# Kernel tuning notes

Hardware: AMD Instinct MI355X
Metric: run time of the kernel (lower is better)

The kernel has to match this reference:

```python
import jax, jax.numpy as jnp
import numpy as np

B, L, D = 4, 4096, 1024
H = 16
HD = D // H                      # 64
WIN = 256
MLP_RATIO = 4.0
FFN = int(2 * int(D * MLP_RATIO) / 3)   # 2730
EPS = 1e-6


def setup_inputs() -> dict:
    key = jax.random.key(0)
    ks = jax.random.split(key, 16)
    s = 0.02
    return {
        "x": jax.random.normal(ks[0], (B, L, D), jnp.float32),
        "c": jax.random.normal(ks[1], (B, D), jnp.float32),
        "norm1_scale": jnp.ones((D,), jnp.float32),
        "norm2_scale": jnp.ones((D,), jnp.float32),
        "adaLN_w": jax.random.normal(ks[2], (D, 6 * D), jnp.float32) * s,
        "adaLN_b": jnp.zeros((6 * D,), jnp.float32),
        "qkv_w": jax.random.normal(ks[3], (D, 3 * D), jnp.float32) * s,
        "qkv_b": jnp.zeros((3 * D,), jnp.float32),
        "out_proj_w": jax.random.normal(ks[4], (D, D), jnp.float32) * s,
        "out_proj_b": jnp.zeros((D,), jnp.float32),
        "w12_w": jax.random.normal(ks[5], (D, 2 * FFN), jnp.float32) * s,
        "w12_b": jnp.zeros((2 * FFN,), jnp.float32),
        "w3_w": jax.random.normal(ks[6], (FFN, D), jnp.float32) * s,
        "w3_b": jnp.zeros((D,), jnp.float32),
    }


def _rmsnorm(x, scale):
    xf = x.astype(jnp.float32)
    var = jnp.mean(jnp.square(xf), axis=-1, keepdims=True)
    xn = (xf * jax.lax.rsqrt(var + EPS)).astype(x.dtype)
    return xn * scale


def _modulation(x, shift, scale):
    return x * (1.0 + scale[:, None, :]) + shift[:, None, :]


def _rope(x):
    # Faithful to original: seq axis is x.shape[-2], which here is the HEAD axis.
    seq_len, hd = x.shape[-2], x.shape[-1]
    theta = 10000.0
    freqs = 1.0 / theta ** (jnp.arange(0, hd, 2, dtype=jnp.float32) / hd)
    t = jnp.arange(seq_len, dtype=jnp.float32)
    freqs_cis = jnp.einsum("i,j->ij", t, freqs)        # (seq, hd/2)
    sin = jnp.repeat(jnp.sin(freqs_cis), 2, axis=-1)   # (seq, hd)
    cos = jnp.repeat(jnp.cos(freqs_cis), 2, axis=-1)
    x1, x2 = jnp.split(x, 2, axis=-1)
    rot = jnp.concatenate([-x2, x1], axis=-1)
    return x * cos + rot * sin


def reference(x, c, norm1_scale, norm2_scale, adaLN_w, adaLN_b,
              qkv_w, qkv_b, out_proj_w, out_proj_b,
              w12_w, w12_b, w3_w, w3_b):
    # adaLN modulation params from conditioning
    ada = jax.nn.silu(c) @ adaLN_w + adaLN_b                      # (B, 6D)
    sh_msa, sc_msa, g_msa, sh_mlp, sc_mlp, g_mlp = jnp.split(ada, 6, axis=-1)

    # --- attention branch ---
    res = x
    xm = _modulation(_rmsnorm(x, norm1_scale), sh_msa, sc_msa)    # (B,L,D)
    nw = L // WIN
    xw = xm.reshape(B * nw, WIN, D)
    qkv = xw @ qkv_w + qkv_b
    q, k, v = jnp.split(qkv, 3, axis=-1)
    q = q.reshape(B * nw, WIN, H, HD)
    k = k.reshape(B * nw, WIN, H, HD)
    v = v.reshape(B * nw, WIN, H, HD)
    q, k = _rope(q), _rope(k)
    scores = jnp.einsum("bqhd,bkhd->bhqk", q, k) / jnp.sqrt(jnp.float32(HD))
    attn = jax.nn.softmax(scores, axis=-1)
    out = jnp.einsum("bhqk,bkhd->bqhd", attn, v).reshape(B, L, D)
    out = out @ out_proj_w + out_proj_b
    x = res + g_msa[:, None, :] * out

    # --- MLP branch ---
    res = x
    xm = _modulation(_rmsnorm(x, norm2_scale), sh_mlp, sc_mlp)
    w12 = xm @ w12_w + w12_b                                      # (B,L,2*FFN)
    w1, w2 = jnp.split(w12, 2, axis=-1)
    mlp = (jax.nn.silu(w1) * w2) @ w3_w + w3_b
    return res + g_mlp[:, None, :] * mlp
```

## Files before the change

### kernel.cpp

```cpp
#include <hip/hip_runtime.h>
#include <hip/hip_bf16.h>
#include <cstdint>
#include <cstddef>

#define DEV __device__ __forceinline__

typedef float f32x4 __attribute__((ext_vector_type(4)));
typedef short s16x8 __attribute__((ext_vector_type(8)));
typedef short s16x4 __attribute__((ext_vector_type(4)));
typedef __bf16 bf16x8 __attribute__((ext_vector_type(8)));

DEV unsigned short f2bf(float f) {
  union { float f; unsigned u; } v; v.f = f;
  return (unsigned short)((v.u + 0x7FFFu + ((v.u >> 16) & 1u)) >> 16);
}
DEV float bf2f(unsigned short s) {
  union { unsigned u; float f; } v; v.u = ((unsigned)s) << 16;
  return v.f;
}

DEV void mfma16(f32x4& d, const s16x8& a, const s16x8& b) {
  d = __builtin_amdgcn_mfma_f32_16x16x32_bf16(
      __builtin_bit_cast(bf16x8, a), __builtin_bit_cast(bf16x8, b), d, 0, 0, 0);
}

typedef const unsigned int gu32 __attribute__((address_space(1)));
typedef unsigned int lu32 __attribute__((address_space(3)));
DEV void gl_lds16(const void* g, void* l) {
  __builtin_amdgcn_global_load_lds((gu32*)g, (lu32*)l, 16, 0, 0);
}

__global__ void transpose_w(const float* __restrict__ src, int srcLd, int K,
                            int colOff, int nCols,
                            unsigned short* __restrict__ dst, int dstLd, int rowOff,
                            int ilv)
{
  __shared__ float tile[32][33];
  int tx = threadIdx.x & 31, ty = threadIdx.x >> 5;
  int k0 = blockIdx.y * 32, n0 = blockIdx.x * 32;
#pragma unroll
  for (int r = 0; r < 4; ++r) {
    int kk = k0 + ty + r * 8;
    int nn = n0 + tx;
    if (kk < K && nn < nCols) tile[ty + r * 8][tx] = src[(size_t)kk * srcLd + colOff + nn];
  }
  __syncthreads();
#pragma unroll
  for (int r = 0; r < 4; ++r) {
    int nn = n0 + ty + r * 8;
    int kk = k0 + tx;
    if (nn < nCols && kk < K) {
      int row = ilv ? (((nn >> 4) << 5) + (nn & 15) + rowOff) : (rowOff + nn);
      dst[(size_t)row * dstLd + kk] = f2bf(tile[tx][ty + r * 8]);
    }
  }
}

__global__ void biaspad_kernel(const float* __restrict__ b, float* __restrict__ out)
{
  int n = blockIdx.x * 256 + threadIdx.x;
  if (n >= 5632) return;
  int bb = n >> 4, i = n & 15;
  int src = ((bb >> 1) << 4) + i;
  float v = 0.f;
  if (src < 2730) v = (bb & 1) ? b[2730 + src] : b[src];
  out[n] = v;
}

__global__ void ada_kernel(const float* __restrict__ c, const float* __restrict__ w,
                           const float* __restrict__ b, float* __restrict__ ada)
{
  __shared__ float cs[1024];
  int bb = blockIdx.y;
  int j = blockIdx.x * 256 + threadIdx.x;
  for (int i = threadIdx.x; i < 1024; i += 256) {
    float v = c[bb * 1024 + i];
    cs[i] = v / (1.f + __expf(-v));
  }
  __syncthreads();
  float acc = b[j];
  for (int k = 0; k < 1024; ++k) acc = fmaf(cs[k], w[(size_t)k * 6144 + j], acc);
  ada[bb * 6144 + j] = acc;
}

__global__ void rmsmod_kernel(const float* __restrict__ x, const float* __restrict__ nsc,
                              const float* __restrict__ ada, int shOff, int scOff,
                              unsigned short* __restrict__ out)
{
  int row = blockIdx.x;
  int t = threadIdx.x;
  const f32x4* xr = (const f32x4*)(x + (size_t)row * 1024);
  f32x4 v = xr[t];
  float ss = v[0]*v[0] + v[1]*v[1] + v[2]*v[2] + v[3]*v[3];
#pragma unroll
  for (int off = 32; off >= 1; off >>= 1) ss += __shfl_xor(ss, off, 64);
  __shared__ float red[4];
  int lane = t & 63, wv = t >> 6;
  if (lane == 0) red[wv] = ss;
  __syncthreads();
  float tot = red[0] + red[1] + red[2] + red[3];
  float rms = rsqrtf(tot * (1.f / 1024.f) + 1e-6f);
  int bb = row >> 12;
  const float* ab = ada + bb * 6144;
  s16x4 o;
#pragma unroll
  for (int i = 0; i < 4; ++i) {
    int col = t * 4 + i;
    float xn = v[i] * rms * nsc[col];
    float val = xn * (1.f + ab[scOff + col]) + ab[shOff + col];
    o[i] = (short)f2bf(val);
  }
  *(s16x4*)(out + (size_t)row * 1024 + t * 4) = o;
}

template<int EPI>
__global__ __launch_bounds__(512, 2) void gemm256(
    const unsigned short* __restrict__ A, int lda,
    const unsigned short* __restrict__ BT, int ldb,
    int N, int K,
    const float* __restrict__ bias,
    void* __restrict__ Cout, int Nout,
    const float* __restrict__ res,
    const float* __restrict__ ada, int gateOff,
    unsigned short* __restrict__ vTout)
{
  __shared__ __align__(16) char lds[131072];

  const int tid = threadIdx.x;
  const int lane = tid & 63;
  const int wv = tid >> 6;
  const int wr = wv >> 2;
  const int wn = wv & 3;
  const int g = lane >> 4, r16 = lane & 15;

  const int nwg = gridDim.x * gridDim.y;
  const int bid = blockIdx.x + gridDim.x * blockIdx.y;
  const int qq = nwg >> 3;
  const int swz = (bid & 7) * qq + (bid >> 3);
  const int m0 = (swz / gridDim.x) * 256;
  const int n0 = (swz % gridDim.x) * 256;

  const int nkt = K >> 6;

  auto stageB = [&](int t) {
    if (t >= nkt) return;
    const int bs = t & 1;
#pragma unroll
    for (int it = 0; it < 4; ++it) {
      const int cidx = it * 512 + tid;
      const int rl = cidx >> 3, cc = cidx & 7;
      const unsigned short* src =
          BT + (size_t)(n0 + rl) * ldb + t * 64 + ((cc ^ (rl & 7)) << 3);
      gl_lds16(src, lds + 65536 + bs * 32768 + cidx * 16);
    }
  };
  auto stageA = [&](int t) {
    if (t >= nkt) return;
    const int bs = t & 1;
#pragma unroll
    for (int it = 0; it < 4; ++it) {
      const int cidx = it * 512 + tid;
      const int rl = cidx >> 3, cc = cidx & 7;
      const unsigned short* src =
          A + (size_t)(m0 + rl) * lda + t * 64 + ((cc ^ (rl & 7)) << 3);
      gl_lds16(src, lds + bs * 32768 + cidx * 16);
    }
  };

  f32x4 acc[8][4];
#pragma unroll
  for (int m = 0; m < 8; ++m)
#pragma unroll
    for (int n = 0; n < 4; ++n) { acc[m][n][0]=0.f; acc[m][n][1]=0.f; acc[m][n][2]=0.f; acc[m][n][3]=0.f; }

  int swzk[2];
#pragma unroll
  for (int ks = 0; ks < 2; ++ks) swzk[ks] = (((ks << 2) + g) ^ (r16 & 7)) << 4;
  int arow0[4], arow1[4], brow0[2], brow1[2];
#pragma unroll
  for (int m = 0; m < 4; ++m) {
    arow0[m] = (wr * 128 + m * 16 + r16) * 128;
    arow1[m] = (wr * 128 + 64 + m * 16 + r16) * 128;
  }
#pragma unroll
  for (int n = 0; n < 2; ++n) {
    brow0[n] = 65536 + (wn * 64 + n * 16 + r16) * 128;
    brow1[n] = 65536 + (wn * 64 + 32 + n * 16 + r16) * 128;
  }

  stageB(0); stageA(0); stageB(1); stageA(1);
  asm volatile("s_waitcnt vmcnt(8)" ::: "memory");
  __builtin_amdgcn_s_barrier();

  for (int kt = 0; kt < nkt; ++kt) {
    const int boff = (kt & 1) * 32768;
    s16x8 a0[4][2], a1[4][2], b0[2][2], b1[2][2];
#pragma unroll
    for (int m = 0; m < 4; ++m)
#pragma unroll
      for (int ks = 0; ks < 2; ++ks)
        a0[m][ks] = *(const s16x8*)(lds + boff + arow0[m] + swzk[ks]);
#pragma unroll
    for (int n = 0; n < 2; ++n)
#pragma unroll
      for (int ks = 0; ks < 2; ++ks)
        b0[n][ks] = *(const s16x8*)(lds + boff + brow0[n] + swzk[ks]);
#pragma unroll
    for (int n = 0; n < 2; ++n)
#pragma unroll
      for (int ks = 0; ks < 2; ++ks)
        b1[n][ks] = *(const s16x8*)(lds + boff + brow1[n] + swzk[ks]);
#pragma unroll
    for (int m = 0; m < 4; ++m)
#pragma unroll
      for (int ks = 0; ks < 2; ++ks)
        a1[m][ks] = *(const s16x8*)(lds + boff + arow1[m] + swzk[ks]);
    __builtin_amdgcn_s_setprio(1);
#pragma unroll
    for (int m = 0; m < 4; ++m)
#pragma unroll
      for (int n = 0; n < 2; ++n)
#pragma unroll
        for (int ks = 0; ks < 2; ++ks)
          mfma16(acc[m][n], a0[m][ks], b0[n][ks]);
    __builtin_amdgcn_s_setprio(0);
    __builtin_amdgcn_s_setprio(1);
#pragma unroll
    for (int m = 0; m < 4; ++m)
#pragma unroll
      for (int n = 0; n < 2; ++n)
#pragma unroll
        for (int ks = 0; ks < 2; ++ks)
          mfma16(acc[m][2 + n], a0[m][ks], b1[n][ks]);
    __builtin_amdgcn_s_setprio(0);
    __builtin_amdgcn_s_barrier();
    stageB(kt + 2);
    __builtin_amdgcn_s_setprio(1);
#pragma unroll
    for (int m = 0; m < 4; ++m)
#pragma unroll
      for (int n = 0; n < 2; ++n)
#pragma unroll
        for (int ks = 0; ks < 2; ++ks)
          mfma16(acc[4 + m][2 + n], a1[m][ks], b1[n][ks]);
    __builtin_amdgcn_s_setprio(0);
    if (kt + 2 < nkt) asm volatile("s_waitcnt vmcnt(4)" ::: "memory");
    else              asm volatile("s_waitcnt vmcnt(0)" ::: "memory");
    __builtin_amdgcn_s_barrier();
    stageA(kt + 2);
    __builtin_amdgcn_s_setprio(1);
#pragma unroll
    for (int m = 0; m < 4; ++m)
#pragma unroll
      for (int n = 0; n < 2; ++n)
#pragma unroll
        for (int ks = 0; ks < 2; ++ks)
          mfma16(acc[4 + m][n], a1[m][ks], b0[n][ks]);
    __builtin_amdgcn_s_setprio(0);
  }

  if (EPI == 1) {
    unsigned short* Co = (unsigned short*)Cout;
#pragma unroll
    for (int fm = 0; fm < 8; ++fm)
#pragma unroll
      for (int p = 0; p < 2; ++p)
#pragma unroll
        for (int r = 0; r < 4; ++r) {
          int rg = m0 + wr * 128 + fm * 16 + g * 4 + r;
          int cg = n0 + wn * 64 + (2 * p) * 16 + r16;
          float v1 = acc[fm][2 * p][r] + bias[cg];
          float v2 = acc[fm][2 * p + 1][r] + bias[cg + 16];
          float h = v1 / (1.f + __expf(-v1)) * v2;
          int hcol = (n0 >> 1) + wn * 32 + p * 16 + r16;
          Co[(size_t)rg * Nout + hcol] = f2bf(h);
        }
  } else if (EPI == 2) {
    float* Co = (float*)Cout;
#pragma unroll
    for (int fm = 0; fm < 8; ++fm)
#pragma unroll
      for (int fn = 0; fn < 4; ++fn)
#pragma unroll
        for (int r = 0; r < 4; ++r) {
          int rg = m0 + wr * 128 + fm * 16 + g * 4 + r;
          int cg = n0 + wn * 64 + fn * 16 + r16;
          float v = acc[fm][fn][r] + bias[cg];
          int bb = rg >> 12;
          float gate = ada[bb * 6144 + gateOff + cg];
          size_t idx = (size_t)rg * Nout + cg;
          Co[idx] = res[idx] + gate * v;
        }
  } else {
    unsigned short* Co = (unsigned short*)Cout;
#pragma unroll
    for (int fn = 0; fn < 4; ++fn) {
      int cg = n0 + wn * 64 + fn * 16 + r16;
      float bs = bias[cg];
      if (n0 + wn * 64 + fn * 16 < 2048) {
#pragma unroll
        for (int fm = 0; fm < 8; ++fm)
#pragma unroll
          for (int r = 0; r < 4; ++r) {
            int rg = m0 + wr * 128 + fm * 16 + g * 4 + r;
            Co[(size_t)rg * Nout + cg] = f2bf(acc[fm][fn][r] + bs);
          }
      } else {
        int h = (cg - 2048) >> 6, d = (cg - 2048) & 63;
        unsigned short* vcol = vTout + (size_t)h * 16384 + d * 256;
#pragma unroll
        for (int fm = 0; fm < 8; ++fm)
#pragma unroll
          for (int r = 0; r < 4; ++r) {
            int rg = m0 + wr * 128 + fm * 16 + g * 4 + r;
            vcol[((size_t)(rg >> 8) * 16) * 16384 + (rg & 255)] =
                f2bf(acc[fm][fn][r] + bs);
          }
      }
    }
  }
}

template<int MODE>
__global__ void gemm128(const unsigned short* __restrict__ A, int lda,
                        const unsigned short* __restrict__ BT,
                        int N, int K,
                        const float* __restrict__ bias,
                        void* __restrict__ Cout,
                        const float* __restrict__ res,
                        const float* __restrict__ ada, int gateOff, int mOff)
{
  __shared__ __align__(16) unsigned short As[128 * 32];
  __shared__ __align__(16) unsigned short Bs[128 * 32];

  const int tid = threadIdx.x;
  const int lane = tid & 63;
  const int wv = tid >> 6;
  const int wr = wv >> 1, wc = wv & 1;
  const int g = lane >> 4, r16 = lane & 15;
  const int m0 = blockIdx.y * 128, n0 = blockIdx.x * 128;

  const int c0 = tid, c1 = 256 + tid;
  const int ra0 = c0 >> 2, ra1 = c1 >> 2;
  const int k0 = ((c0 & 3) ^ ((ra0 >> 1) & 3)) * 8;
  const int k1 = ((c1 & 3) ^ ((ra1 >> 1) & 3)) * 8;
  const unsigned short* ga0 = A + (size_t)(m0 + ra0) * lda + k0;
  const unsigned short* ga1 = A + (size_t)(m0 + ra1) * lda + k1;
  const unsigned short* gb0 = BT + (size_t)(n0 + ra0) * K + k0;
  const unsigned short* gb1 = BT + (size_t)(n0 + ra1) * K + k1;
  unsigned short* la0 = As + c0 * 8;
  unsigned short* la1 = As + c1 * 8;
  unsigned short* lb0 = Bs + c0 * 8;
  unsigned short* lb1 = Bs + c1 * 8;

  f32x4 acc[4][4];
#pragma unroll
  for (int m = 0; m < 4; ++m)
#pragma unroll
    for (int n = 0; n < 4; ++n) { acc[m][n][0]=0.f; acc[m][n][1]=0.f; acc[m][n][2]=0.f; acc[m][n][3]=0.f; }

  int aoff[4], boff[4];
#pragma unroll
  for (int m = 0; m < 4; ++m) {
    int rl = wr * 64 + m * 16 + r16;
    aoff[m] = rl * 32 + (g ^ ((rl >> 1) & 3)) * 8;
    int rb = wc * 64 + m * 16 + r16;
    boff[m] = rb * 32 + (g ^ ((rb >> 1) & 3)) * 8;
  }

  const int nk = K >> 5;
  for (int kt = 0; kt < nk; ++kt) {
    __syncthreads();
    const int ko = kt * 32;
    gl_lds16(ga0 + ko, la0);
    gl_lds16(ga1 + ko, la1);
    gl_lds16(gb0 + ko, lb0);
    gl_lds16(gb1 + ko, lb1);
    __syncthreads();
    s16x8 af[4], bf[4];
#pragma unroll
    for (int m = 0; m < 4; ++m) af[m] = *(const s16x8*)(As + aoff[m]);
#pragma unroll
    for (int n = 0; n < 4; ++n) bf[n] = *(const s16x8*)(Bs + boff[n]);
#pragma unroll
    for (int m = 0; m < 4; ++m)
#pragma unroll
      for (int n = 0; n < 4; ++n) mfma16(acc[m][n], af[m], bf[n]);
  }

#pragma unroll
  for (int m = 0; m < 4; ++m) {
#pragma unroll
    for (int n = 0; n < 4; ++n) {
#pragma unroll
      for (int r = 0; r < 4; ++r) {
        int rg = m0 + wr * 64 + m * 16 + g * 4 + r;
        int cg = n0 + wc * 64 + n * 16 + r16;
        float v = acc[m][n][r] + bias[cg];
        size_t idx = (size_t)rg * N + cg;
        if (MODE == 0 || MODE == 2) {
          ((unsigned short*)Cout)[idx] = f2bf(v);
        } else {
          int bb = (mOff + rg) >> 12;
          float gate = ada[bb * 6144 + gateOff + cg];
          ((float*)Cout)[idx] = res[idx] + gate * v;
        }
      }
    }
  }
}

__global__ __launch_bounds__(256, 1) void attn_kernel(
    const unsigned short* __restrict__ qkv,
    const unsigned short* __restrict__ vT,
    unsigned short* __restrict__ attnout)
{
  __shared__ __align__(16) unsigned short Kl[256 * 64];
  __shared__ __align__(16) unsigned short Vl[64 * 256];
  __shared__ __align__(16) unsigned short Pl[4][64 * 88];

  const int tid = threadIdx.x;
  const int lane = tid & 63;
  const int wv = tid >> 6;
  const int g = lane >> 4, r16 = lane & 15;
  const int p = blockIdx.x;
  const int w = p >> 4, h = p & 15;
  const float hh = (float)h;
  const float F = 0.4152410118609203f;

#pragma unroll
  for (int it = 0; it < 4; ++it) {
    int idx = it * 256 + tid;
    int j = idx >> 2;
    int c = idx & 3;
    const unsigned short* kg = qkv + (size_t)(w * 256 + j) * 3072 + 1024 + h * 64;
    s16x8 lo = *(const s16x8*)(kg + c * 8);
    s16x8 hi = *(const s16x8*)(kg + 32 + c * 8);
    s16x8 plo, phi;
#pragma unroll
    for (int i2 = 0; i2 < 4; ++i2) {
      float f1 = exp2f(-(float)(c * 4 + i2) * F);
      float f2 = exp2f(-(float)(16 + c * 4 + i2) * F);
      float s1, c1s, s2, c2s;
      sincosf(hh * f1, &s1, &c1s);
      sincosf(hh * f2, &s2, &c2s);
#pragma unroll
      for (int u = 0; u < 2; ++u) {
        int i = i2 * 2 + u;
        float a = bf2f((unsigned short)lo[i]);
        float b = bf2f((unsigned short)hi[i]);
        plo[i] = (short)f2bf(a * c1s - b * s1);
        phi[i] = (short)f2bf(b * c2s + a * s2);
      }
    }
    int swzL = c ^ (j & 7);
    int swzH = (c + 4) ^ (j & 7);
    *(s16x8*)(Kl + j * 64 + swzL * 8) = plo;
    *(s16x8*)(Kl + j * 64 + swzH * 8) = phi;
  }
  {
    const unsigned short* vg = vT + (size_t)p * (64 * 256);
#pragma unroll
    for (int it = 0; it < 8; ++it) {
      int idx = it * 256 + tid;
      int d = idx >> 5;
      int c = idx & 31;
      s16x8 val = *(const s16x8*)(vg + d * 256 + c * 8);
      int cs = (c & ~7) | ((c ^ d) & 7);
      *(s16x8*)(Vl + d * 256 + cs * 8) = val;
    }
  }

  s16x8 qa[4][2];
  {
    float cs0[4], sn0[4], cs1[4], sn1[4];
#pragma unroll
    for (int i2 = 0; i2 < 4; ++i2) {
      float f1 = exp2f(-(float)(g * 4 + i2) * F);
      float f2 = exp2f(-(float)(16 + g * 4 + i2) * F);
      sincosf(hh * f1, &sn0[i2], &cs0[i2]);
      sincosf(hh * f2, &sn1[i2], &cs1[i2]);
    }
#pragma unroll
    for (int m = 0; m < 4; ++m) {
      const unsigned short* qg =
          qkv + (size_t)(w * 256 + wv * 64 + m * 16 + r16) * 3072 + h * 64;
      s16x8 lo = *(const s16x8*)(qg + g * 8);
      s16x8 hi = *(const s16x8*)(qg + 32 + g * 8);
      s16x8 plo, phi;
#pragma unroll
      for (int i = 0; i < 8; ++i) {
        int i2 = i >> 1;
        float a = bf2f((unsigned short)lo[i]);
        float b = bf2f((unsigned short)hi[i]);
        plo[i] = (short)f2bf(a * cs0[i2] - b * sn0[i2]);
        phi[i] = (short)f2bf(b * cs1[i2] + a * sn1[i2]);
      }
      qa[m][0] = plo;
      qa[m][1] = phi;
    }
  }

  __syncthreads();

  f32x4 accO[4][4];
  float Mx[4][4], Ls[4][4];
#pragma unroll
  for (int m = 0; m < 4; ++m)
#pragma unroll
    for (int r = 0; r < 4; ++r) {
      Mx[m][r] = -3.0e38f;
      Ls[m][r] = 0.f;
      accO[m][r][0]=0.f; accO[m][r][1]=0.f; accO[m][r][2]=0.f; accO[m][r][3]=0.f;
    }
  unsigned short* Pw = &Pl[wv][0];
  const float zs = 0.125f * 1.44269504f;

  for (int kb = 0; kb < 4; ++kb) {
    f32x4 s[4][4];
#pragma unroll
    for (int m = 0; m < 4; ++m)
#pragma unroll
      for (int jt = 0; jt < 4; ++jt) { s[m][jt][0]=0.f; s[m][jt][1]=0.f; s[m][jt][2]=0.f; s[m][jt][3]=0.f; }

#pragma unroll
    for (int jt = 0; jt < 4; ++jt) {
      int j = kb * 64 + jt * 16 + r16;
      s16x8 bk0 = *(const s16x8*)(Kl + j * 64 + ((g ^ (j & 7)) * 8));
      s16x8 bk1 = *(const s16x8*)(Kl + j * 64 + (((4 + g) ^ (j & 7)) * 8));
#pragma unroll
      for (int m = 0; m < 4; ++m) {
        mfma16(s[m][jt], qa[m][0], bk0);
        mfma16(s[m][jt], qa[m][1], bk1);
      }
    }

#pragma unroll
    for (int m = 0; m < 4; ++m) {
#pragma unroll
      for (int r = 0; r < 4; ++r) {
        float mx = fmaxf(fmaxf(s[m][0][r], s[m][1][r]), fmaxf(s[m][2][r], s[m][3][r]));
        mx = fmaxf(mx, __shfl_xor(mx, 1, 16));
        mx = fmaxf(mx, __shfl_xor(mx, 2, 16));
        mx = fmaxf(mx, __shfl_xor(mx, 4, 16));
        mx = fmaxf(mx, __shfl_xor(mx, 8, 16));
        float Mn = fmaxf(Mx[m][r], mx * zs);
        float fsc = exp2f(Mx[m][r] - Mn);
        Mx[m][r] = Mn;
        float ps = 0.f;
#pragma unroll
        for (int jt = 0; jt < 4; ++jt) {
          float pv = exp2f(s[m][jt][r] * zs - Mn);
          s[m][jt][r] = pv;
          ps += pv;
        }
        ps += __shfl_xor(ps, 1, 16);
        ps += __shfl_xor(ps, 2, 16);
        ps += __shfl_xor(ps, 4, 16);
        ps += __shfl_xor(ps, 8, 16);
        Ls[m][r] = Ls[m][r] * fsc + ps;
#pragma unroll
        for (int dt = 0; dt < 4; ++dt) accO[m][dt][r] *= fsc;
      }
    }

#pragma unroll
    for (int m = 0; m < 4; ++m)
#pragma unroll
      for (int jt = 0; jt < 4; ++jt)
#pragma unroll
        for (int r = 0; r < 4; ++r) {
          int q = m * 16 + g * 4 + r;
          int jj = jt * 16 + r16;
          Pw[q * 88 + jj] = f2bf(s[m][jt][r]);
        }
    asm volatile("s_waitcnt lgkmcnt(0)" ::: "memory");
    __builtin_amdgcn_sched_barrier(0);

#pragma unroll
    for (int c = 0; c < 2; ++c) {
      s16x8 pa[4];
#pragma unroll
      for (int m = 0; m < 4; ++m)
        pa[m] = *(const s16x8*)(Pw + (m * 16 + r16) * 88 + c * 32 + g * 8);
#pragma unroll
      for (int dt = 0; dt < 4; ++dt) {
        int d = dt * 16 + r16;
        int cch = kb * 8 + c * 4 + g;
        int csz = (cch & ~7) | ((cch ^ d) & 7);
        s16x8 vb = *(const s16x8*)(Vl + d * 256 + csz * 8);
#pragma unroll
        for (int m = 0; m < 4; ++m) mfma16(accO[m][dt], pa[m], vb);
      }
    }
    asm volatile("s_waitcnt lgkmcnt(0)" ::: "memory");
    __builtin_amdgcn_sched_barrier(0);
  }

#pragma unroll
  for (int m = 0; m < 4; ++m)
#pragma unroll
    for (int dt = 0; dt < 4; ++dt)
#pragma unroll
      for (int r = 0; r < 4; ++r) {
        int rg = w * 256 + wv * 64 + m * 16 + g * 4 + r;
        int cg = h * 64 + dt * 16 + r16;
        float val = accO[m][dt][r] / Ls[m][r];
        attnout[(size_t)rg * 1024 + cg] = f2bf(val);
      }
}

extern "C" void kernel_launch(void* const* d_in, const int* in_sizes, int n_in,
                              void* d_out, int out_size, void* d_ws, size_t ws_size,
                              hipStream_t stream)
{
  const float* x    = (const float*)d_in[0];
  const float* c    = (const float*)d_in[1];
  const float* n1s  = (const float*)d_in[2];
  const float* n2s  = (const float*)d_in[3];
  const float* adaW = (const float*)d_in[4];
  const float* adaB = (const float*)d_in[5];
  const float* qkvW = (const float*)d_in[6];
  const float* qkvB = (const float*)d_in[7];
  const float* outW = (const float*)d_in[8];
  const float* outB = (const float*)d_in[9];
  const float* w12W = (const float*)d_in[10];
  const float* w12B = (const float*)d_in[11];
  const float* w3W  = (const float*)d_in[12];
  const float* w3B  = (const float*)d_in[13];

  char* ws = (char*)d_ws;
  constexpr size_t OFF_ADA  = 0;
  constexpr size_t OFF_QKVT = 98304;
  constexpr size_t OFF_OUTT = OFF_QKVT + 6291456;
  constexpr size_t OFF_W12T = OFF_OUTT + 2097152;
  constexpr size_t OFF_W3T  = OFF_W12T + 11534336;
  constexpr size_t OFF_BPAD = OFF_W3T + 5767168;
  constexpr size_t OFF_XM   = OFF_BPAD + 22528;
  constexpr size_t OFF_BIG  = OFF_XM + 33554432;
  constexpr size_t OFF_QKVC = OFF_BIG;
  constexpr size_t OFF_VTC  = OFF_BIG + 50331648;
  constexpr size_t OFF_ATTC = OFF_BIG + 67108864;
  constexpr size_t OFF_HBUF = OFF_BIG;

  float* ada            = (float*)(ws + OFF_ADA);
  unsigned short* qkvT  = (unsigned short*)(ws + OFF_QKVT);
  unsigned short* outT  = (unsigned short*)(ws + OFF_OUTT);
  unsigned short* w12T  = (unsigned short*)(ws + OFF_W12T);
  unsigned short* w3T   = (unsigned short*)(ws + OFF_W3T);
  float* biasPad        = (float*)(ws + OFF_BPAD);
  unsigned short* xm    = (unsigned short*)(ws + OFF_XM);
  unsigned short* qkvbC = (unsigned short*)(ws + OFF_QKVC);
  unsigned short* vTbC  = (unsigned short*)(ws + OFF_VTC);
  unsigned short* attnC = (unsigned short*)(ws + OFF_ATTC);
  unsigned short* hbuf  = (unsigned short*)(ws + OFF_HBUF);
  float* x2             = (float*)d_out;

  hipMemsetAsync(w12T, 0, 11534336, stream);
  hipMemsetAsync(w3T, 0, 5767168, stream);
  transpose_w<<<dim3(96, 32), 256, 0, stream>>>(qkvW, 3072, 1024, 0, 3072, qkvT, 1024, 0, 0);
  transpose_w<<<dim3(32, 32), 256, 0, stream>>>(outW, 1024, 1024, 0, 1024, outT, 1024, 0, 0);
  transpose_w<<<dim3(86, 32), 256, 0, stream>>>(w12W, 5460, 1024, 0, 2730, w12T, 1024, 0, 1);
  transpose_w<<<dim3(86, 32), 256, 0, stream>>>(w12W, 5460, 1024, 2730, 2730, w12T, 1024, 16, 1);
  transpose_w<<<dim3(32, 86), 256, 0, stream>>>(w3W, 1024, 2730, 0, 1024, w3T, 2816, 0, 0);
  biaspad_kernel<<<22, 256, 0, stream>>>(w12B, biasPad);
  ada_kernel<<<dim3(24, 4), 256, 0, stream>>>(c, adaW, adaB, ada);

  rmsmod_kernel<<<16384, 256, 0, stream>>>(x, n1s, ada, 0, 1024, xm);
  for (int ch = 0; ch < 2; ++ch) {
    const size_t ro = (size_t)ch * 8192;
    gemm256<3><<<dim3(12, 32), 512, 0, stream>>>(
        xm + ro * 1024, 1024, qkvT, 1024, 3072, 1024, qkvB, qkvbC, 3072,
        nullptr, nullptr, 0, vTbC);
    attn_kernel<<<512, 256, 0, stream>>>(qkvbC, vTbC, attnC);
    gemm128<1><<<dim3(8, 64), 256, 0, stream>>>(
        attnC, 1024, outT, 1024, 1024, outB, x2 + ro * 1024, x + ro * 1024,
        ada, 2048, (int)ro);
  }

  rmsmod_kernel<<<16384, 256, 0, stream>>>(x2, n2s, ada, 3072, 4096, xm);
  gemm256<1><<<dim3(22, 64), 512, 0, stream>>>(
      xm, 1024, w12T, 1024, 5632, 1024, biasPad, hbuf, 2816,
      nullptr, nullptr, 0, nullptr);
  gemm256<2><<<dim3(4, 64), 512, 0, stream>>>(
      hbuf, 2816, w3T, 2816, 1024, 2816, w3B, x2, 1024,
      x2, ada, 5120, nullptr);
}
```

Before: 765.9 us.

## Interleave LDS fragment reads and global staging with MFMA phases in GEMM loop

Restructures the GEMM main loop so the b1 and a1 LDS fragment loads happen just before the MFMA phase that uses them, rather than all up front. Each phase is bracketed by barriers and lgkmcnt waits. Global-to-LDS staging is split into two 128-row halves, and the vmcnt wait moves to the end of each iteration. The aim is to cut register pressure and overlap LDS and global traffic with matrix work. The cost is several extra workgroup barriers per K-step, which could stall the waves.

```diff
diff --git a/kernel.cpp b/kernel.cpp
--- a/kernel.cpp
+++ b/kernel.cpp
@@ -142,28 +142,30 @@
 
   const int nkt = K >> 6;
 
-  auto stageB = [&](int t) {
+  auto stageBh = [&](int t, int h) {
     if (t >= nkt) return;
     const int bs = t & 1;
 #pragma unroll
-    for (int it = 0; it < 4; ++it) {
+    for (int it = 0; it < 2; ++it) {
       const int cidx = it * 512 + tid;
       const int rl = cidx >> 3, cc = cidx & 7;
+      const int row = h * 128 + rl;
       const unsigned short* src =
-          BT + (size_t)(n0 + rl) * ldb + t * 64 + ((cc ^ (rl & 7)) << 3);
-      gl_lds16(src, lds + 65536 + bs * 32768 + cidx * 16);
+          BT + (size_t)(n0 + row) * ldb + t * 64 + ((cc ^ (rl & 7)) << 3);
+      gl_lds16(src, lds + 65536 + bs * 32768 + h * 16384 + cidx * 16);
     }
   };
-  auto stageA = [&](int t) {
+  auto stageAh = [&](int t, int h) {
     if (t >= nkt) return;
     const int bs = t & 1;
 #pragma unroll
-    for (int it = 0; it < 4; ++it) {
+    for (int it = 0; it < 2; ++it) {
       const int cidx = it * 512 + tid;
       const int rl = cidx >> 3, cc = cidx & 7;
+      const int row = h * 128 + rl;
       const unsigned short* src =
-          A + (size_t)(m0 + rl) * lda + t * 64 + ((cc ^ (rl & 7)) << 3);
-      gl_lds16(src, lds + bs * 32768 + cidx * 16);
+          A + (size_t)(m0 + row) * lda + t * 64 + ((cc ^ (rl & 7)) << 3);
+      gl_lds16(src, lds + bs * 32768 + h * 16384 + cidx * 16);
     }
   };
 
@@ -188,7 +190,8 @@
     brow1[n] = 65536 + (wn * 64 + 32 + n * 16 + r16) * 128;
   }
 
-  stageB(0); stageA(0); stageB(1); stageA(1);
+  stageBh(0, 0); stageBh(0, 1); stageAh(0, 0); stageAh(0, 1);
+  stageBh(1, 0); stageBh(1, 1); stageAh(1, 0); stageAh(1, 1);
   asm volatile("s_waitcnt vmcnt(8)" ::: "memory");
   __builtin_amdgcn_s_barrier();
 
@@ -205,16 +208,8 @@
 #pragma unroll
       for (int ks = 0; ks < 2; ++ks)
         b0[n][ks] = *(const s16x8*)(lds + boff + brow0[n] + swzk[ks]);
-#pragma unroll
-    for (int n = 0; n < 2; ++n)
-#pragma unroll
-      for (int ks = 0; ks < 2; ++ks)
-        b1[n][ks] = *(const s16x8*)(lds + boff + brow1[n] + swzk[ks]);
-#pragma unroll
-    for (int m = 0; m < 4; ++m)
-#pragma unroll
-      for (int ks = 0; ks < 2; ++ks)
-        a1[m][ks] = *(const s16x8*)(lds + boff + arow1[m] + swzk[ks]);
+    __builtin_amdgcn_s_barrier();
+    asm volatile("s_waitcnt lgkmcnt(0)" ::: "memory");
     __builtin_amdgcn_s_setprio(1);
 #pragma unroll
     for (int m = 0; m < 4; ++m)
@@ -224,6 +219,14 @@
         for (int ks = 0; ks < 2; ++ks)
           mfma16(acc[m][n], a0[m][ks], b0[n][ks]);
     __builtin_amdgcn_s_setprio(0);
+    __builtin_amdgcn_s_barrier();
+#pragma unroll
+    for (int n = 0; n < 2; ++n)
+#pragma unroll
+      for (int ks = 0; ks < 2; ++ks)
+        b1[n][ks] = *(const s16x8*)(lds + boff + brow1[n] + swzk[ks]);
+    __builtin_amdgcn_s_barrier();
+    asm volatile("s_waitcnt lgkmcnt(0)" ::: "memory");
     __builtin_amdgcn_s_setprio(1);
 #pragma unroll
     for (int m = 0; m < 4; ++m)
@@ -234,7 +237,15 @@
           mfma16(acc[m][2 + n], a0[m][ks], b1[n][ks]);
     __builtin_amdgcn_s_setprio(0);
     __builtin_amdgcn_s_barrier();
-    stageB(kt + 2);
+#pragma unroll
+    for (int m = 0; m < 4; ++m)
+#pragma unroll
+      for (int ks = 0; ks < 2; ++ks)
+        a1[m][ks] = *(const s16x8*)(lds + boff + arow1[m] + swzk[ks]);
+    stageBh(kt + 2, 0);
+    stageBh(kt + 2, 1);
+    __builtin_amdgcn_s_barrier();
+    asm volatile("s_waitcnt lgkmcnt(0)" ::: "memory");
     __builtin_amdgcn_s_setprio(1);
 #pragma unroll
     for (int m = 0; m < 4; ++m)
@@ -244,10 +255,10 @@
         for (int ks = 0; ks < 2; ++ks)
           mfma16(acc[4 + m][2 + n], a1[m][ks], b1[n][ks]);
     __builtin_amdgcn_s_setprio(0);
-    if (kt + 2 < nkt) asm volatile("s_waitcnt vmcnt(4)" ::: "memory");
-    else              asm volatile("s_waitcnt vmcnt(0)" ::: "memory");
     __builtin_amdgcn_s_barrier();
-    stageA(kt + 2);
+    stageAh(kt + 2, 0);
+    stageAh(kt + 2, 1);
+    __builtin_amdgcn_s_barrier();
     __builtin_amdgcn_s_setprio(1);
 #pragma unroll
     for (int m = 0; m < 4; ++m)
@@ -257,6 +268,8 @@
         for (int ks = 0; ks < 2; ++ks)
           mfma16(acc[4 + m][n], a1[m][ks], b0[n][ks]);
     __builtin_amdgcn_s_setprio(0);
+    asm volatile("s_waitcnt vmcnt(8)" ::: "memory");
+    __builtin_amdgcn_s_barrier();
   }
 
   if (EPI == 1) {
```

After: 805.7 us. 5.2% more time.

## Shrink gemm256 tile to 256x128 with K-step 32 for higher occupancy

Applied to the files above, without the earlier changes.

Reworks the main bf16 GEMM from a 256x256 tile with K-step 64 to a 256x128 tile with K-step 32. The wave layout changes to 4x2, each wave holds a 64x64 accumulator, and LDS drops from 128KB to 48KB. The launch bound rises to 4 blocks per CU and grid widths double. The goal is more resident workgroups and better wave balance across CUs, at the cost of lower arithmetic intensity per LDS byte, more barriers per K, and more global traffic for the A operand.

```diff
diff --git a/kernel.cpp b/kernel.cpp
--- a/kernel.cpp
+++ b/kernel.cpp
@@ -114,7 +114,7 @@
 }
 
 template<int EPI>
-__global__ __launch_bounds__(512, 2) void gemm256(
+__global__ __launch_bounds__(512, 4) void gemm256(
     const unsigned short* __restrict__ A, int lda,
     const unsigned short* __restrict__ BT, int ldb,
     int N, int K,
@@ -124,13 +124,13 @@
     const float* __restrict__ ada, int gateOff,
     unsigned short* __restrict__ vTout)
 {
-  __shared__ __align__(16) char lds[131072];
+  __shared__ __align__(16) char lds[49152];
 
   const int tid = threadIdx.x;
   const int lane = tid & 63;
   const int wv = tid >> 6;
-  const int wr = wv >> 2;
-  const int wn = wv & 3;
+  const int wr = wv >> 1;
+  const int wn = wv & 1;
   const int g = lane >> 4, r16 = lane & 15;
 
   const int nwg = gridDim.x * gridDim.y;
@@ -138,136 +138,85 @@
   const int qq = nwg >> 3;
   const int swz = (bid & 7) * qq + (bid >> 3);
   const int m0 = (swz / gridDim.x) * 256;
-  const int n0 = (swz % gridDim.x) * 256;
-
-  const int nkt = K >> 6;
+  const int n0 = (swz % gridDim.x) * 128;
+
+  const int nkt = K >> 5;
 
   auto stageB = [&](int t) {
     if (t >= nkt) return;
     const int bs = t & 1;
-#pragma unroll
-    for (int it = 0; it < 4; ++it) {
-      const int cidx = it * 512 + tid;
-      const int rl = cidx >> 3, cc = cidx & 7;
-      const unsigned short* src =
-          BT + (size_t)(n0 + rl) * ldb + t * 64 + ((cc ^ (rl & 7)) << 3);
-      gl_lds16(src, lds + 65536 + bs * 32768 + cidx * 16);
-    }
+    const int rl = tid >> 2, cc = tid & 3;
+    const unsigned short* src =
+        BT + (size_t)(n0 + rl) * ldb + t * 32 + ((cc ^ ((rl >> 1) & 3)) << 3);
+    gl_lds16(src, lds + 32768 + bs * 8192 + tid * 16);
   };
   auto stageA = [&](int t) {
     if (t >= nkt) return;
     const int bs = t & 1;
 #pragma unroll
-    for (int it = 0; it < 4; ++it) {
+    for (int it = 0; it < 2; ++it) {
       const int cidx = it * 512 + tid;
-      const int rl = cidx >> 3, cc = cidx & 7;
+      const int rl = cidx >> 2, cc = cidx & 3;
       const unsigned short* src =
-          A + (size_t)(m0 + rl) * lda + t * 64 + ((cc ^ (rl & 7)) << 3);
-      gl_lds16(src, lds + bs * 32768 + cidx * 16);
+          A + (size_t)(m0 + rl) * lda + t * 32 + ((cc ^ ((rl >> 1) & 3)) << 3);
+      gl_lds16(src, lds + bs * 16384 + cidx * 16);
     }
   };
 
-  f32x4 acc[8][4];
-#pragma unroll
-  for (int m = 0; m < 8; ++m)
+  f32x4 acc[4][4];
+#pragma unroll
+  for (int m = 0; m < 4; ++m)
 #pragma unroll
     for (int n = 0; n < 4; ++n) { acc[m][n][0]=0.f; acc[m][n][1]=0.f; acc[m][n][2]=0.f; acc[m][n][3]=0.f; }
 
-  int swzk[2];
-#pragma unroll
-  for (int ks = 0; ks < 2; ++ks) swzk[ks] = (((ks << 2) + g) ^ (r16 & 7)) << 4;
-  int arow0[4], arow1[4], brow0[2], brow1[2];
-#pragma unroll
-  for (int m = 0; m < 4; ++m) {
-    arow0[m] = (wr * 128 + m * 16 + r16) * 128;
-    arow1[m] = (wr * 128 + 64 + m * 16 + r16) * 128;
-  }
-#pragma unroll
-  for (int n = 0; n < 2; ++n) {
-    brow0[n] = 65536 + (wn * 64 + n * 16 + r16) * 128;
-    brow1[n] = 65536 + (wn * 64 + 32 + n * 16 + r16) * 128;
-  }
+  const int swzc = (g ^ ((r16 >> 1) & 3)) << 4;
+  int aoff[4], boff[4];
+#pragma unroll
+  for (int m = 0; m < 4; ++m) aoff[m] = (wr * 64 + m * 16 + r16) * 64 + swzc;
+#pragma unroll
+  for (int n = 0; n < 4; ++n) boff[n] = 32768 + (wn * 64 + n * 16 + r16) * 64 + swzc;
 
   stageB(0); stageA(0); stageB(1); stageA(1);
-  asm volatile("s_waitcnt vmcnt(8)" ::: "memory");
+  asm volatile("s_waitcnt vmcnt(3)" ::: "memory");
   __builtin_amdgcn_s_barrier();
 
   for (int kt = 0; kt < nkt; ++kt) {
-    const int boff = (kt & 1) * 32768;
-    s16x8 a0[4][2], a1[4][2], b0[2][2], b1[2][2];
-#pragma unroll
-    for (int m = 0; m < 4; ++m)
-#pragma unroll
-      for (int ks = 0; ks < 2; ++ks)
-        a0[m][ks] = *(const s16x8*)(lds + boff + arow0[m] + swzk[ks]);
-#pragma unroll
-    for (int n = 0; n < 2; ++n)
-#pragma unroll
-      for (int ks = 0; ks < 2; ++ks)
-        b0[n][ks] = *(const s16x8*)(lds + boff + brow0[n] + swzk[ks]);
-#pragma unroll
-    for (int n = 0; n < 2; ++n)
-#pragma unroll
-      for (int ks = 0; ks < 2; ++ks)
-        b1[n][ks] = *(const s16x8*)(lds + boff + brow1[n] + swzk[ks]);
-#pragma unroll
-    for (int m = 0; m < 4; ++m)
-#pragma unroll
-      for (int ks = 0; ks < 2; ++ks)
-        a1[m][ks] = *(const s16x8*)(lds + boff + arow1[m] + swzk[ks]);
+    const int aboff = (kt & 1) * 16384;
+    const int bboff = (kt & 1) * 8192;
+    s16x8 af[4], bf[4];
+#pragma unroll
+    for (int m = 0; m < 4; ++m) af[m] = *(const s16x8*)(lds + aboff + aoff[m]);
+#pragma unroll
+    for (int n = 0; n < 4; ++n) bf[n] = *(const s16x8*)(lds + bboff + boff[n]);
     __builtin_amdgcn_s_setprio(1);
 #pragma unroll
-    for (int m = 0; m < 4; ++m)
-#pragma unroll
-      for (int n = 0; n < 2; ++n)
-#pragma unroll
-        for (int ks = 0; ks < 2; ++ks)
-          mfma16(acc[m][n], a0[m][ks], b0[n][ks]);
-    __builtin_amdgcn_s_setprio(0);
-    __builtin_amdgcn_s_setprio(1);
-#pragma unroll
-    for (int m = 0; m < 4; ++m)
-#pragma unroll
-      for (int n = 0; n < 2; ++n)
-#pragma unroll
-        for (int ks = 0; ks < 2; ++ks)
-          mfma16(acc[m][2 + n], a0[m][ks], b1[n][ks]);
+    for (int m = 0; m < 2; ++m)
+#pragma unroll
+      for (int n = 0; n < 4; ++n) mfma16(acc[m][n], af[m], bf[n]);
     __builtin_amdgcn_s_setprio(0);
     __builtin_amdgcn_s_barrier();
     stageB(kt + 2);
     __builtin_amdgcn_s_setprio(1);
 #pragma unroll
-    for (int m = 0; m < 4; ++m)
-#pragma unroll
-      for (int n = 0; n < 2; ++n)
-#pragma unroll
-        for (int ks = 0; ks < 2; ++ks)
-          mfma16(acc[4 + m][2 + n], a1[m][ks], b1[n][ks]);
+    for (int m = 2; m < 4; ++m)
+#pragma unroll
+      for (int n = 0; n < 4; ++n) mfma16(acc[m][n], af[m], bf[n]);
     __builtin_amdgcn_s_setprio(0);
-    if (kt + 2 < nkt) asm volatile("s_waitcnt vmcnt(4)" ::: "memory");
+    if (kt + 2 < nkt) asm volatile("s_waitcnt vmcnt(1)" ::: "memory");
     else              asm volatile("s_waitcnt vmcnt(0)" ::: "memory");
     __builtin_amdgcn_s_barrier();
     stageA(kt + 2);
-    __builtin_amdgcn_s_setprio(1);
-#pragma unroll
-    for (int m = 0; m < 4; ++m)
-#pragma unroll
-      for (int n = 0; n < 2; ++n)
-#pragma unroll
-        for (int ks = 0; ks < 2; ++ks)
-          mfma16(acc[4 + m][n], a1[m][ks], b0[n][ks]);
-    __builtin_amdgcn_s_setprio(0);
   }
 
   if (EPI == 1) {
     unsigned short* Co = (unsigned short*)Cout;
 #pragma unroll
-    for (int fm = 0; fm < 8; ++fm)
+    for (int fm = 0; fm < 4; ++fm)
 #pragma unroll
       for (int p = 0; p < 2; ++p)
 #pragma unroll
         for (int r = 0; r < 4; ++r) {
-          int rg = m0 + wr * 128 + fm * 16 + g * 4 + r;
+          int rg = m0 + wr * 64 + fm * 16 + g * 4 + r;
           int cg = n0 + wn * 64 + (2 * p) * 16 + r16;
           float v1 = acc[fm][2 * p][r] + bias[cg];
           float v2 = acc[fm][2 * p + 1][r] + bias[cg + 16];
@@ -278,12 +227,12 @@
   } else if (EPI == 2) {
     float* Co = (float*)Cout;
 #pragma unroll
-    for (int fm = 0; fm < 8; ++fm)
+    for (int fm = 0; fm < 4; ++fm)
 #pragma unroll
       for (int fn = 0; fn < 4; ++fn)
 #pragma unroll
         for (int r = 0; r < 4; ++r) {
-          int rg = m0 + wr * 128 + fm * 16 + g * 4 + r;
+          int rg = m0 + wr * 64 + fm * 16 + g * 4 + r;
           int cg = n0 + wn * 64 + fn * 16 + r16;
           float v = acc[fm][fn][r] + bias[cg];
           int bb = rg >> 12;
@@ -299,20 +248,20 @@
       float bs = bias[cg];
       if (n0 + wn * 64 + fn * 16 < 2048) {
 #pragma unroll
-        for (int fm = 0; fm < 8; ++fm)
+        for (int fm = 0; fm < 4; ++fm)
 #pragma unroll
           for (int r = 0; r < 4; ++r) {
-            int rg = m0 + wr * 128 + fm * 16 + g * 4 + r;
+            int rg = m0 + wr * 64 + fm * 16 + g * 4 + r;
             Co[(size_t)rg * Nout + cg] = f2bf(acc[fm][fn][r] + bs);
           }
       } else {
         int h = (cg - 2048) >> 6, d = (cg - 2048) & 63;
         unsigned short* vcol = vTout + (size_t)h * 16384 + d * 256;
 #pragma unroll
-        for (int fm = 0; fm < 8; ++fm)
+        for (int fm = 0; fm < 4; ++fm)
 #pragma unroll
           for (int r = 0; r < 4; ++r) {
-            int rg = m0 + wr * 128 + fm * 16 + g * 4 + r;
+            int rg = m0 + wr * 64 + fm * 16 + g * 4 + r;
             vcol[((size_t)(rg >> 8) * 16) * 16384 + (rg & 255)] =
                 f2bf(acc[fm][fn][r] + bs);
           }
@@ -669,7 +618,7 @@
   rmsmod_kernel<<<16384, 256, 0, stream>>>(x, n1s, ada, 0, 1024, xm);
   for (int ch = 0; ch < 2; ++ch) {
     const size_t ro = (size_t)ch * 8192;
-    gemm256<3><<<dim3(12, 32), 512, 0, stream>>>(
+    gemm256<3><<<dim3(24, 32), 512, 0, stream>>>(
         xm + ro * 1024, 1024, qkvT, 1024, 3072, 1024, qkvB, qkvbC, 3072,
         nullptr, nullptr, 0, vTbC);
     attn_kernel<<<512, 256, 0, stream>>>(qkvbC, vTbC, attnC);
@@ -679,10 +628,10 @@
   }
 
   rmsmod_kernel<<<16384, 256, 0, stream>>>(x2, n2s, ada, 3072, 4096, xm);
-  gemm256<1><<<dim3(22, 64), 512, 0, stream>>>(
+  gemm256<1><<<dim3(44, 64), 512, 0, stream>>>(
       xm, 1024, w12T, 1024, 5632, 1024, biasPad, hbuf, 2816,
       nullptr, nullptr, 0, nullptr);
-  gemm256<2><<<dim3(4, 64), 512, 0, stream>>>(
+  gemm256<2><<<dim3(8, 64), 512, 0, stream>>>(
       hbuf, 2816, w3T, 2816, 1024, 2816, w3B, x2, 1024,
       x2, ada, 5120, nullptr);
 }
```

Result: no change. 775.7 us (+1.3%).
